# Optimization experiments

Measured on AMD Instinct MI355X. Metric: run time of the kernel, lower is better.

The kernel has to match this reference:

```python
import jax, jax.numpy as jnp
import numpy as np


def setup_inputs() -> dict:
    key = jax.random.key(0)
    ks = jax.random.split(key, 6)
    B, C, H, W = 8, 64, 64, 64
    E = C // 8  # embedding_channels = inChannels // k
    inp = {
        "x": jax.random.normal(ks[0], (B, C, H, W), dtype=jnp.float32),
        "Wk": jax.random.normal(ks[1], (E, C), dtype=jnp.float32) * 0.1,
        "bk": jnp.zeros((E,), dtype=jnp.float32),
        "Wq": jax.random.normal(ks[2], (E, C), dtype=jnp.float32) * 0.1,
        "bq": jnp.zeros((E,), dtype=jnp.float32),
        "Wv": jax.random.normal(ks[3], (E, C), dtype=jnp.float32) * 0.1,
        "bv": jnp.zeros((E,), dtype=jnp.float32),
        "Wo": jax.random.normal(ks[4], (C, E), dtype=jnp.float32) * 0.1,
        "bo": jnp.zeros((C,), dtype=jnp.float32),
        "gamma": jnp.zeros((1,), dtype=jnp.float32),
    }
    return inp


def reference(x, Wk, bk, Wq, bq, Wv, bv, Wo, bo, gamma):
    B, C, H, W = x.shape
    N = H * W
    xf = x.reshape(B, C, N)  # [B, C, N]
    # 1x1 convs are per-pixel linear projections
    f = jnp.einsum('ec,bcn->ben', Wk, xf) + bk[:, None]  # key   [B, E, N]
    g = jnp.einsum('ec,bcn->ben', Wq, xf) + bq[:, None]  # query [B, E, N]
    h = jnp.einsum('ec,bcn->ben', Wv, xf) + bv[:, None]  # value [B, E, N]
    # s = f^T g : [B, N, N]
    s = jnp.einsum('ben,bem->bnm', f, g)
    # softmax over dim=1 (key/row axis) as in the original module
    beta = jax.nn.softmax(s, axis=1)
    v = jnp.einsum('ben,bnm->bem', h, beta)  # [B, E, N]
    o = jnp.einsum('ce,ben->bcn', Wo, v) + bo[:, None]  # [B, C, N]
    o = o.reshape(B, C, H, W)
    y = gamma[0] * o + x
    return (y, o, gamma[0])
```

## Files before the change

kernel.cpp:

```cpp
#include <hip/hip_runtime.h>


#define BB   8
#define CC   64
#define NPIX 4096
#define EE   8
#define BN   (BB*NPIX)
#define YSZ  (BB*CC*NPIX)
#define LOG2E 1.4426950408889634f

typedef __attribute__((ext_vector_type(8))) short bf16x8;
typedef __attribute__((ext_vector_type(4))) float f32x4;

__device__ __forceinline__ unsigned short f2bf_rne(float x) {
    unsigned u = __float_as_uint(x);
    u += 0x7FFFu + ((u >> 16) & 1u);
    return (unsigned short)(u >> 16);
}
__device__ __forceinline__ unsigned pack_bf_trunc(float a, float b) {
    return (__float_as_uint(a) >> 16) | (__float_as_uint(b) & 0xFFFF0000u);
}

__global__ __launch_bounds__(256) void qkv_kernel(
    const float* __restrict__ x,
    const float* __restrict__ Wk, const float* __restrict__ bk,
    const float* __restrict__ Wq, const float* __restrict__ bq,
    const float* __restrict__ Wv, const float* __restrict__ bv,
    unsigned short* __restrict__ QT, unsigned short* __restrict__ KT,
    unsigned short* __restrict__ VT)
{
    const int proj = blockIdx.y;
    const float* W    = (proj == 0) ? Wq : (proj == 1) ? Wk : Wv;
    const float* bias = (proj == 0) ? bq : (proj == 1) ? bk : bv;

    const int bm = blockIdx.x*256 + threadIdx.x;
    const int b  = bm >> 12;
    const int n  = bm & (NPIX-1);
    const float* xb = x + (size_t)b*CC*NPIX + n;

    float xv[CC];
    #pragma unroll
    for (int c = 0; c < CC; ++c) xv[c] = xb[(size_t)c*NPIX];

    float f[EE];
    #pragma unroll
    for (int e = 0; e < EE; ++e) {
        float acc = bias[e];
        #pragma unroll
        for (int c = 0; c < CC; ++c) acc = fmaf(W[e*CC+c], xv[c], acc);
        f[e] = acc;
    }

    if (proj == 0) {
        union { unsigned short s[8]; uint4 v; } t;
        #pragma unroll
        for (int e = 0; e < EE; ++e) t.s[e] = f2bf_rne(f[e] * LOG2E);
        *(uint4*)(QT + (size_t)bm*EE) = t.v;
    } else if (proj == 1) {
        union { unsigned short s[8]; uint4 v; } t;
        #pragma unroll
        for (int e = 0; e < EE; ++e) t.s[e] = f2bf_rne(f[e]);
        *(uint4*)(KT + (size_t)bm*EE) = t.v;
    } else {
        #pragma unroll
        for (int e = 0; e < EE; ++e)
            VT[((size_t)b*16 + e)*NPIX + n] = f2bf_rne(f[e]);
    }
}

__global__ __launch_bounds__(256) void attn_fused(
    const unsigned short* __restrict__ QT, const unsigned short* __restrict__ KT,
    const unsigned short* __restrict__ VT,
    const float* __restrict__ x, const float* __restrict__ Wo,
    const float* __restrict__ bo, const float* __restrict__ gamma,
    float* __restrict__ out)
{
    __shared__ float OB[3*2*256];
    __shared__ float LB[3*2*16];
    __shared__ float VL[32*8];
    __shared__ float Wos[CC*9];
    __shared__ float bos[CC];

    const int tid  = threadIdx.x;
    const int wave = tid >> 6, lane = tid & 63;
    const int quad = lane >> 4, lm = lane & 15;
    const int b  = blockIdx.x >> 7;
    const int m0 = (blockIdx.x & 127) * 32;

    for (int i = tid; i < CC*EE; i += 256) Wos[(i>>3)*9 + (i&7)] = Wo[i];
    if (tid < CC) bos[tid] = bo[tid];

    bf16x8 qfA = {0,0,0,0,0,0,0,0}, qfB = {0,0,0,0,0,0,0,0};
    if (quad == 0) {
        qfA = *(const bf16x8*)(QT + (size_t)(b*NPIX + m0 + lm)*EE);
        qfB = *(const bf16x8*)(QT + (size_t)(b*NPIX + m0 + 16 + lm)*EE);
    }

    f32x4 oaccA = {0.f,0.f,0.f,0.f}, oaccB = {0.f,0.f,0.f,0.f};
    const f32x4 zc = {0.f,0.f,0.f,0.f};
    float laccA = 0.f, laccB = 0.f;

    const unsigned short* Kb = KT + (size_t)b*NPIX*EE;
    const unsigned short* Vb = VT + (size_t)b*16*NPIX;
    const int n_start = wave*1024;
    const unsigned short* kl  = Kb + (size_t)(n_start + lm)*EE;
    const unsigned short* vlA = Vb + (size_t)lm*NPIX + n_start + quad*4;

    bf16x8 kf0n = {0,0,0,0,0,0,0,0}, kf1n = {0,0,0,0,0,0,0,0};
    if (quad == 0) {
        kf0n = *(const bf16x8*)(kl);
        kf1n = *(const bf16x8*)(kl + 16*EE);
    }
    uint2 vf0n = *(const uint2*)(vlA);
    uint2 vf1n = *(const uint2*)(vlA + 16);

    for (int ch = 0; ch < 32; ++ch) {
        bf16x8 kf0 = kf0n, kf1 = kf1n;
        union { unsigned short s[8]; bf16x8 v; uint2 h[2]; } vf;
        vf.h[0] = vf0n; vf.h[1] = vf1n;
        kl += 32*EE; vlA += 32;
        if (ch < 31) {
            if (quad == 0) {
                kf0n = *(const bf16x8*)(kl);
                kf1n = *(const bf16x8*)(kl + 16*EE);
            }
            vf0n = *(const uint2*)(vlA);
            vf1n = *(const uint2*)(vlA + 16);
        }

        f32x4 s0a = __builtin_amdgcn_mfma_f32_16x16x32_bf16(kf0, qfA, zc, 0, 0, 0);
        f32x4 s1a = __builtin_amdgcn_mfma_f32_16x16x32_bf16(kf1, qfA, zc, 0, 0, 0);
        f32x4 s0b = __builtin_amdgcn_mfma_f32_16x16x32_bf16(kf0, qfB, zc, 0, 0, 0);
        f32x4 s1b = __builtin_amdgcn_mfma_f32_16x16x32_bf16(kf1, qfB, zc, 0, 0, 0);

        float a0 = __builtin_amdgcn_exp2f(s0a.x), a1 = __builtin_amdgcn_exp2f(s0a.y);
        float a2 = __builtin_amdgcn_exp2f(s0a.z), a3 = __builtin_amdgcn_exp2f(s0a.w);
        float a4 = __builtin_amdgcn_exp2f(s1a.x), a5 = __builtin_amdgcn_exp2f(s1a.y);
        float a6 = __builtin_amdgcn_exp2f(s1a.z), a7 = __builtin_amdgcn_exp2f(s1a.w);
        float b0 = __builtin_amdgcn_exp2f(s0b.x), b1 = __builtin_amdgcn_exp2f(s0b.y);
        float b2 = __builtin_amdgcn_exp2f(s0b.z), b3 = __builtin_amdgcn_exp2f(s0b.w);
        float b4 = __builtin_amdgcn_exp2f(s1b.x), b5 = __builtin_amdgcn_exp2f(s1b.y);
        float b6 = __builtin_amdgcn_exp2f(s1b.z), b7 = __builtin_amdgcn_exp2f(s1b.w);
        laccA += ((a0+a1)+(a2+a3)) + ((a4+a5)+(a6+a7));
        laccB += ((b0+b1)+(b2+b3)) + ((b4+b5)+(b6+b7));

        union { unsigned u[4]; bf16x8 v; } puA, puB;
        puA.u[0] = pack_bf_trunc(a0, a1); puA.u[1] = pack_bf_trunc(a2, a3);
        puA.u[2] = pack_bf_trunc(a4, a5); puA.u[3] = pack_bf_trunc(a6, a7);
        puB.u[0] = pack_bf_trunc(b0, b1); puB.u[1] = pack_bf_trunc(b2, b3);
        puB.u[2] = pack_bf_trunc(b4, b5); puB.u[3] = pack_bf_trunc(b6, b7);
        oaccA = __builtin_amdgcn_mfma_f32_16x16x32_bf16(vf.v, puA.v, oaccA, 0, 0, 0);
        oaccB = __builtin_amdgcn_mfma_f32_16x16x32_bf16(vf.v, puB.v, oaccB, 0, 0, 0);
    }

    laccA += __shfl_xor(laccA, 16); laccA += __shfl_xor(laccA, 32);
    laccB += __shfl_xor(laccB, 16); laccB += __shfl_xor(laccB, 32);

    if (wave != 0) {
        *(f32x4*)(OB + ((size_t)(wave-1)*2 + 0)*256 + lane*4) = oaccA;
        *(f32x4*)(OB + ((size_t)(wave-1)*2 + 1)*256 + lane*4) = oaccB;
        if (lane < 16) {
            LB[((wave-1)*2 + 0)*16 + lane] = laccA;
            LB[((wave-1)*2 + 1)*16 + lane] = laccB;
        }
    }
    __syncthreads();
    if (wave == 0) {
        f32x4 oA = oaccA, oB = oaccB;
        float lA = laccA, lB = laccB;
        #pragma unroll
        for (int w = 0; w < 3; ++w) {
            oA += *(f32x4*)(OB + ((size_t)w*2 + 0)*256 + lane*4);
            oB += *(f32x4*)(OB + ((size_t)w*2 + 1)*256 + lane*4);
            lA += LB[(w*2 + 0)*16 + lm];
            lB += LB[(w*2 + 1)*16 + lm];
        }
        float invA = 1.f / lA, invB = 1.f / lB;
        if (quad < 2) {
            f32x4 sA = { oA.x*invA, oA.y*invA, oA.z*invA, oA.w*invA };
            f32x4 sB = { oB.x*invB, oB.y*invB, oB.z*invB, oB.w*invB };
            *(f32x4*)(VL + lm*8 + quad*4)        = sA;
            *(f32x4*)(VL + (16 + lm)*8 + quad*4) = sB;
        }
    }
    __syncthreads();

    const float g  = gamma[0];
    const int   px = tid & 31;
    const int   cg = tid >> 5;
    const size_t base = (size_t)b*CC*NPIX + (m0 + px);
    float v[EE];
    #pragma unroll
    for (int e = 0; e < EE; ++e) v[e] = VL[px*8 + e];
    #pragma unroll
    for (int i = 0; i < 8; ++i) {
        const int c = cg*8 + i;
        float o = bos[c];
        #pragma unroll
        for (int e = 0; e < EE; ++e) o += Wos[c*9 + e] * v[e];
        out[(size_t)YSZ + base + (size_t)c*NPIX] = o;
        out[base + (size_t)c*NPIX] = g*o + x[base + (size_t)c*NPIX];
    }
    if (blockIdx.x == 0 && tid == 0) out[2*(size_t)YSZ] = g;
}

extern "C" void kernel_launch(void* const* d_in, const int* in_sizes, int n_in,
                              void* d_out, int out_size, void* d_ws, size_t ws_size,
                              hipStream_t stream) {
    const float* x     = (const float*)d_in[0];
    const float* Wk    = (const float*)d_in[1];
    const float* bk    = (const float*)d_in[2];
    const float* Wq    = (const float*)d_in[3];
    const float* bq    = (const float*)d_in[4];
    const float* Wv    = (const float*)d_in[5];
    const float* bv    = (const float*)d_in[6];
    const float* Wo    = (const float*)d_in[7];
    const float* bo    = (const float*)d_in[8];
    const float* gamma = (const float*)d_in[9];
    float* out = (float*)d_out;

    unsigned short* QT = (unsigned short*)d_ws;
    unsigned short* KT = QT + (size_t)BN*EE;
    unsigned short* VT = KT + (size_t)BN*EE;

    qkv_kernel<<<dim3(BN/256, 3), 256, 0, stream>>>(x, Wk, bk, Wq, bq, Wv, bv, QT, KT, VT);
    attn_fused<<<BB*128, 256, 0, stream>>>(QT, KT, VT, x, Wo, bo, gamma, out);
}
```

Before: 131.2 us.

## Fold softmax denominator into PV MFMA via ones row and retile V layout

New measurement: 111.1 us. 1.18x faster.

```diff
diff --git a/kernel.cpp b/kernel.cpp
--- a/kernel.cpp
+++ b/kernel.cpp
@@ -18,7 +18,8 @@
     return (unsigned short)(u >> 16);
 }
 __device__ __forceinline__ unsigned pack_bf_trunc(float a, float b) {
-    return (__float_as_uint(a) >> 16) | (__float_as_uint(b) & 0xFFFF0000u);
+    return __builtin_amdgcn_perm(__float_as_uint(b), __float_as_uint(a),
+                                 0x07060302u);
 }
 
 __global__ __launch_bounds__(256) void qkv_kernel(
@@ -62,13 +63,17 @@
         for (int e = 0; e < EE; ++e) t.s[e] = f2bf_rne(f[e]);
         *(uint4*)(KT + (size_t)bm*EE) = t.v;
     } else {
-        #pragma unroll
-        for (int e = 0; e < EE; ++e)
-            VT[((size_t)b*16 + e)*NPIX + n] = f2bf_rne(f[e]);
-    }
-}
-
-__global__ __launch_bounds__(256) void attn_fused(
+        const int p   = n >> 5;
+        const int c   = n & 31;
+        const int off = ((c & 15) >> 2)*8 + ((c >> 4) << 2) + (c & 3);
+        unsigned short* vp = VT + ((size_t)(b*128 + p)*16)*32 + off;
+        #pragma unroll
+        for (int e = 0; e < EE; ++e) vp[e*32] = f2bf_rne(f[e]);
+        vp[8*32] = 0x3F80;
+    }
+}
+
+__global__ __launch_bounds__(256, 4) void attn_fused(
     const unsigned short* __restrict__ QT, const unsigned short* __restrict__ KT,
     const unsigned short* __restrict__ VT,
     const float* __restrict__ x, const float* __restrict__ Wo,
@@ -76,8 +81,7 @@
     float* __restrict__ out)
 {
     __shared__ float OB[3*2*256];
-    __shared__ float LB[3*2*16];
-    __shared__ float VL[32*8];
+    __shared__ float VL[32*12];
     __shared__ float Wos[CC*9];
     __shared__ float bos[CC];
 
@@ -98,34 +102,31 @@
 
     f32x4 oaccA = {0.f,0.f,0.f,0.f}, oaccB = {0.f,0.f,0.f,0.f};
     const f32x4 zc = {0.f,0.f,0.f,0.f};
-    float laccA = 0.f, laccB = 0.f;
 
     const unsigned short* Kb = KT + (size_t)b*NPIX*EE;
-    const unsigned short* Vb = VT + (size_t)b*16*NPIX;
     const int n_start = wave*1024;
-    const unsigned short* kl  = Kb + (size_t)(n_start + lm)*EE;
-    const unsigned short* vlA = Vb + (size_t)lm*NPIX + n_start + quad*4;
-
-    bf16x8 kf0n = {0,0,0,0,0,0,0,0}, kf1n = {0,0,0,0,0,0,0,0};
-    if (quad == 0) {
-        kf0n = *(const bf16x8*)(kl);
-        kf1n = *(const bf16x8*)(kl + 16*EE);
-    }
-    uint2 vf0n = *(const uint2*)(vlA);
-    uint2 vf1n = *(const uint2*)(vlA + 16);
-
+    const unsigned short* kl = Kb + (size_t)(n_start + lm)*EE;
+    const int lmv = (lm < 9) ? lm : 8;
+    const unsigned short* vl = VT + ((size_t)(b*128 + (n_start >> 5))*16 + lmv)*32
+                                  + quad*8;
+
+    bf16x8 kf0a = *(const bf16x8*)(kl);
+    bf16x8 kf1a = *(const bf16x8*)(kl + 16*EE);
+    bf16x8 vfa  = *(const bf16x8*)(vl);
+    bf16x8 kf0b = *(const bf16x8*)(kl + 32*EE);
+    bf16x8 kf1b = *(const bf16x8*)(kl + 48*EE);
+    bf16x8 vfb  = *(const bf16x8*)(vl + 512);
+    kl += 64*EE; vl += 1024;
+
+    #pragma unroll 2
     for (int ch = 0; ch < 32; ++ch) {
-        bf16x8 kf0 = kf0n, kf1 = kf1n;
-        union { unsigned short s[8]; bf16x8 v; uint2 h[2]; } vf;
-        vf.h[0] = vf0n; vf.h[1] = vf1n;
-        kl += 32*EE; vlA += 32;
-        if (ch < 31) {
-            if (quad == 0) {
-                kf0n = *(const bf16x8*)(kl);
-                kf1n = *(const bf16x8*)(kl + 16*EE);
-            }
-            vf0n = *(const uint2*)(vlA);
-            vf1n = *(const uint2*)(vlA + 16);
+        bf16x8 kf0 = kf0a, kf1 = kf1a, vf = vfa;
+        kf0a = kf0b; kf1a = kf1b; vfa = vfb;
+        if (ch < 30) {
+            kf0b = *(const bf16x8*)(kl);
+            kf1b = *(const bf16x8*)(kl + 16*EE);
+            vfb  = *(const bf16x8*)(vl);
+            kl += 32*EE; vl += 512;
         }
 
         f32x4 s0a = __builtin_amdgcn_mfma_f32_16x16x32_bf16(kf0, qfA, zc, 0, 0, 0);
@@ -141,46 +142,36 @@
         float b2 = __builtin_amdgcn_exp2f(s0b.z), b3 = __builtin_amdgcn_exp2f(s0b.w);
         float b4 = __builtin_amdgcn_exp2f(s1b.x), b5 = __builtin_amdgcn_exp2f(s1b.y);
         float b6 = __builtin_amdgcn_exp2f(s1b.z), b7 = __builtin_amdgcn_exp2f(s1b.w);
-        laccA += ((a0+a1)+(a2+a3)) + ((a4+a5)+(a6+a7));
-        laccB += ((b0+b1)+(b2+b3)) + ((b4+b5)+(b6+b7));
 
         union { unsigned u[4]; bf16x8 v; } puA, puB;
         puA.u[0] = pack_bf_trunc(a0, a1); puA.u[1] = pack_bf_trunc(a2, a3);
         puA.u[2] = pack_bf_trunc(a4, a5); puA.u[3] = pack_bf_trunc(a6, a7);
         puB.u[0] = pack_bf_trunc(b0, b1); puB.u[1] = pack_bf_trunc(b2, b3);
         puB.u[2] = pack_bf_trunc(b4, b5); puB.u[3] = pack_bf_trunc(b6, b7);
-        oaccA = __builtin_amdgcn_mfma_f32_16x16x32_bf16(vf.v, puA.v, oaccA, 0, 0, 0);
-        oaccB = __builtin_amdgcn_mfma_f32_16x16x32_bf16(vf.v, puB.v, oaccB, 0, 0, 0);
-    }
-
-    laccA += __shfl_xor(laccA, 16); laccA += __shfl_xor(laccA, 32);
-    laccB += __shfl_xor(laccB, 16); laccB += __shfl_xor(laccB, 32);
+        oaccA = __builtin_amdgcn_mfma_f32_16x16x32_bf16(vf, puA.v, oaccA, 0, 0, 0);
+        oaccB = __builtin_amdgcn_mfma_f32_16x16x32_bf16(vf, puB.v, oaccB, 0, 0, 0);
+    }
 
     if (wave != 0) {
         *(f32x4*)(OB + ((size_t)(wave-1)*2 + 0)*256 + lane*4) = oaccA;
         *(f32x4*)(OB + ((size_t)(wave-1)*2 + 1)*256 + lane*4) = oaccB;
-        if (lane < 16) {
-            LB[((wave-1)*2 + 0)*16 + lane] = laccA;
-            LB[((wave-1)*2 + 1)*16 + lane] = laccB;
-        }
     }
     __syncthreads();
     if (wave == 0) {
         f32x4 oA = oaccA, oB = oaccB;
-        float lA = laccA, lB = laccB;
         #pragma unroll
         for (int w = 0; w < 3; ++w) {
             oA += *(f32x4*)(OB + ((size_t)w*2 + 0)*256 + lane*4);
             oB += *(f32x4*)(OB + ((size_t)w*2 + 1)*256 + lane*4);
-            lA += LB[(w*2 + 0)*16 + lm];
-            lB += LB[(w*2 + 1)*16 + lm];
         }
+        float lA = __shfl(oA.x, 32 + lm);
+        float lB = __shfl(oB.x, 32 + lm);
         float invA = 1.f / lA, invB = 1.f / lB;
         if (quad < 2) {
             f32x4 sA = { oA.x*invA, oA.y*invA, oA.z*invA, oA.w*invA };
             f32x4 sB = { oB.x*invB, oB.y*invB, oB.z*invB, oB.w*invB };
-            *(f32x4*)(VL + lm*8 + quad*4)        = sA;
-            *(f32x4*)(VL + (16 + lm)*8 + quad*4) = sB;
+            *(f32x4*)(VL + lm*12 + quad*4)        = sA;
+            *(f32x4*)(VL + (16 + lm)*12 + quad*4) = sB;
         }
     }
     __syncthreads();
@@ -191,7 +182,7 @@
     const size_t base = (size_t)b*CC*NPIX + (m0 + px);
     float v[EE];
     #pragma unroll
-    for (int e = 0; e < EE; ++e) v[e] = VL[px*8 + e];
+    for (int e = 0; e < EE; ++e) v[e] = VL[px*12 + e];
     #pragma unroll
     for (int i = 0; i < 8; ++i) {
         const int c = cg*8 + i;
```
